# Kernel optimization log

Measured on AMD Instinct MI355X. Metric: run time of the kernel, lower is better.

The kernel has to match this reference:

```python
import jax, jax.numpy as jnp
import numpy as np

DIM = 1024
HEADS = 16
DIM_HEAD = 64
INNER = HEADS * DIM_HEAD  # 1024
SCALE = DIM_HEAD ** -0.5


def layernorm(x, gamma, beta, eps=1e-5):
    mu = jnp.mean(x, axis=-1, keepdims=True)
    var = jnp.var(x, axis=-1, keepdims=True)
    return (x - mu) * jax.lax.rsqrt(var + eps) * gamma + beta


def setup_inputs() -> dict:
    key = jax.random.key(0)
    ks = jax.random.split(key, 6)
    x = jax.random.normal(ks[0], (2, 2048, DIM), dtype=jnp.float32)
    # params (stored [in, out]; torch Linear does x @ W.T with W [out, in])
    w_q = jax.random.normal(ks[1], (DIM, INNER), dtype=jnp.float32) * (DIM ** -0.5)
    w_kv = jax.random.normal(ks[2], (DIM, 2 * INNER), dtype=jnp.float32) * (DIM ** -0.5)
    w_out = jax.random.normal(ks[3], (INNER, DIM), dtype=jnp.float32) * (INNER ** -0.5)
    b_out = jnp.zeros((DIM,), dtype=jnp.float32)
    gamma = jnp.ones((DIM,), dtype=jnp.float32)
    beta = jnp.zeros((DIM,), dtype=jnp.float32)
    return {"x": x, "w_q": w_q, "w_kv": w_kv, "w_out": w_out, "b_out": b_out,
            "gamma": gamma, "beta": beta}


def reference(x, w_q, w_kv, w_out, b_out, gamma, beta):
    b, n, _ = x.shape
    xn = layernorm(x, gamma, beta)
    q = xn @ w_q                           # [b, n, inner]
    kv = xn @ w_kv                         # [b, n, 2*inner]
    k, v = jnp.split(kv, 2, axis=-1)
    def split_heads(t):
        return t.reshape(b, n, HEADS, DIM_HEAD).transpose(0, 2, 1, 3)  # b h n d
    q, k, v = split_heads(q), split_heads(k), split_heads(v)
    dots = jnp.einsum('bhid,bhjd->bhij', q, k) * SCALE   # [b, h, n, n]
    attn = jax.nn.softmax(dots, axis=-1)
    out = jnp.einsum('bhij,bhjd->bhid', attn, v)          # [b, h, n, d]
    out = out.transpose(0, 2, 1, 3).reshape(b, n, INNER)  # b n (h d)
    return out @ w_out + b_out
```

## Files before the change

### kernel.cpp

```cpp
#include <hip/hip_runtime.h>

typedef unsigned short u16;
typedef u16   u16x8 __attribute__((ext_vector_type(8)));
typedef __bf16 bf16x8 __attribute__((ext_vector_type(8)));
typedef float f32x4 __attribute__((ext_vector_type(4)));
typedef float f32x2 __attribute__((ext_vector_type(2)));
typedef _Float16 f16x4 __attribute__((ext_vector_type(4)));
typedef _Float16 f16x8 __attribute__((ext_vector_type(8)));
typedef unsigned u32x2 __attribute__((ext_vector_type(2)));

__device__ __forceinline__ u16 f2b(float f){ __bf16 h=(__bf16)f; return __builtin_bit_cast(u16,h); }

__device__ __forceinline__ f32x4 mfma16(u16x8 a, u16x8 b, f32x4 c){
  return __builtin_amdgcn_mfma_f32_16x16x32_bf16(
      __builtin_bit_cast(bf16x8,a), __builtin_bit_cast(bf16x8,b), c, 0,0,0);
}

__device__ __forceinline__ void gl2lds16(const u16* g, u16* l){
  __builtin_amdgcn_global_load_lds((const __attribute__((address_space(1))) void*)g,
                                   (__attribute__((address_space(3))) void*)l, 16, 0, 0);
}

__global__ __launch_bounds__(256) void ln_kernel(const float* __restrict__ x,
                                                 const float* __restrict__ gamma,
                                                 const float* __restrict__ beta,
                                                 u16* __restrict__ xn){
  const int row = blockIdx.x, t = threadIdx.x;
  const float4 v = ((const float4*)(x + (size_t)row*1024))[t];
  float s  = v.x+v.y+v.z+v.w;
  float sq = v.x*v.x+v.y*v.y+v.z*v.z+v.w*v.w;
  for (int m=1;m<64;m<<=1){ s += __shfl_xor(s,m); sq += __shfl_xor(sq,m); }
  __shared__ float red[8];
  const int w=t>>6, l=t&63;
  if(l==0){ red[w]=s; red[4+w]=sq; }
  __syncthreads();
  const float S  = red[0]+red[1]+red[2]+red[3];
  const float SQ = red[4]+red[5]+red[6]+red[7];
  const float mu = S*(1.f/1024.f);
  const float var= SQ*(1.f/1024.f)-mu*mu;
  const float rs = rsqrtf(var+1e-5f);
  const float4 g4=((const float4*)gamma)[t], b4=((const float4*)beta)[t];
  u16 o0=f2b((v.x-mu)*rs*g4.x+b4.x);
  u16 o1=f2b((v.y-mu)*rs*g4.y+b4.y);
  u16 o2=f2b((v.z-mu)*rs*g4.z+b4.z);
  u16 o3=f2b((v.w-mu)*rs*g4.w+b4.w);
  uint2 p; p.x=(unsigned)o0|((unsigned)o1<<16); p.y=(unsigned)o2|((unsigned)o3<<16);
  ((uint2*)(xn + (size_t)row*1024))[t]=p;
}

__global__ __launch_bounds__(256) void wtrans_all_kernel(const float* __restrict__ wq,
    const float* __restrict__ wkv, const float* __restrict__ wout,
    u16* __restrict__ wqkvt, u16* __restrict__ woutt){
  __shared__ float tile[64][65];
  const int bx=blockIdx.x, t=threadIdx.x;
  const float* in; u16* out; int C, cxx;
  if(bx<16){ in=wq;  out=wqkvt;           C=1024; cxx=bx; }
  else if(bx<48){ in=wkv; out=wqkvt+1024*1024; C=2048; cxx=bx-16; }
  else { in=wout; out=woutt;             C=1024; cxx=bx-48; }
  const int R=1024;
  const int c0=cxx*64, r0=blockIdx.y*64;
  {
    const int r=t>>2, cc=t&3;
    const float* gp = in + (size_t)(r0+r)*C + c0 + cc*16;
    #pragma unroll
    for(int i=0;i<4;i++){
      float4 f=((const float4*)gp)[i];
      tile[r][cc*16+i*4+0]=f.x; tile[r][cc*16+i*4+1]=f.y;
      tile[r][cc*16+i*4+2]=f.z; tile[r][cc*16+i*4+3]=f.w;
    }
  }
  __syncthreads();
  const int c=t>>2, rc=t&3;
  u16x8 a,b;
  #pragma unroll
  for(int i=0;i<8;i++) a[i]=f2b(tile[rc*16+i][c]);
  #pragma unroll
  for(int i=0;i<8;i++) b[i]=f2b(tile[rc*16+8+i][c]);
  u16* op = out + (size_t)(c0+c)*R + r0 + rc*16;
  *(u16x8*)op=a; *(u16x8*)(op+8)=b;
}

__global__ __launch_bounds__(256) void vpack_kernel(const u16* __restrict__ kv,
                                                    u16* __restrict__ vp){
  __shared__ u16 tile[64][72];
  const int tok0=blockIdx.x*64, h=blockIdx.y, bb=blockIdx.z, t=threadIdx.x;
  {
    const int r=t>>2, cc=t&3;
    const u16* gp = kv + (size_t)(bb*2048 + tok0 + r)*2048 + 1024 + h*64 + cc*16;
    *(u16x8*)&tile[r][cc*16]   = *(const u16x8*)gp;
    *(u16x8*)&tile[r][cc*16+8] = *(const u16x8*)(gp+8);
  }
  __syncthreads();
  const int d=t&63, sl=t>>6;
  #pragma unroll
  for(int pass=0;pass<2;pass++){
    const int combo=pass*4+sl;
    const int j32l=combo>>2, qd=combo&3;
    u16 pk[8];
    #pragma unroll
    for(int tt=0;tt<2;tt++)
      #pragma unroll
      for(int rr=0;rr<4;rr++){
        const unsigned bits=((unsigned)tile[j32l*32+tt*16+qd*4+rr][d])<<16;
        const _Float16 hh=(_Float16)__builtin_bit_cast(float,bits);
        pk[tt*4+rr]=__builtin_bit_cast(u16,hh);
      }
    uint4 w4;
    w4.x=(unsigned)pk[0]|((unsigned)pk[1]<<16); w4.y=(unsigned)pk[2]|((unsigned)pk[3]<<16);
    w4.z=(unsigned)pk[4]|((unsigned)pk[5]<<16); w4.w=(unsigned)pk[6]|((unsigned)pk[7]<<16);
    *(uint4*)&vp[((((size_t)(bb*16+h))*64 + (tok0>>5) + j32l)*4 + qd)*512 + d*8]=w4;
  }
}

template<int MODE,int TM>
__global__ __launch_bounds__(256) void gemm_bt_kernel(const u16* __restrict__ A,
    const u16* __restrict__ Bt, u16* __restrict__ outQ, u16* __restrict__ outKV,
    float* __restrict__ outF, const float* __restrict__ bias, float scale,
    int M, int N, int K){
  constexpr int MT = TM/32;
  __shared__ u16 As[TM*64];
  __shared__ u16 Bs[128*64];
  const int t=threadIdx.x, w=t>>6, l=t&63, qd=l>>4, ln=l&15;
  const int m0=blockIdx.y*TM, n0=blockIdx.x*128;
  const int wm=(w>>1)*(TM/2), wn=(w&1)*64;
  f32x4 acc[MT][4] = {};
  const int nK = K>>6;
  for(int kt=0; kt<nK; kt++){
    const int k0=kt*64;
    #pragma unroll
    for(int p=0;p<MT;p++){
      const int cid=p*256+t, r=cid>>3, pc=cid&7, g=pc^(r&7);
      gl2lds16(A + (size_t)(m0+r)*K + k0 + g*8, &As[(p*256 + (t&192))*8]);
    }
    #pragma unroll
    for(int p=0;p<4;p++){
      const int cid=p*256+t, r=cid>>3, pc=cid&7, g=pc^(r&7);
      gl2lds16(Bt + (size_t)(n0+r)*K + k0 + g*8, &Bs[(p*256 + (t&192))*8]);
    }
    __syncthreads();
    #pragma unroll
    for(int ks=0;ks<2;ks++){
      u16x8 af[MT], bf[4];
      #pragma unroll
      for(int mt=0;mt<MT;mt++){
        const int m=wm+mt*16+ln, kc=ks*4+qd, pcc=kc^(m&7);
        af[mt]=*(const u16x8*)&As[m*64 + pcc*8];
      }
      #pragma unroll
      for(int nt=0;nt<4;nt++){
        const int n=wn+nt*16+ln, kc=ks*4+qd, pcc=kc^(n&7);
        bf[nt]=*(const u16x8*)&Bs[n*64 + pcc*8];
      }
      #pragma unroll
      for(int mt=0;mt<MT;mt++)
        #pragma unroll
        for(int nt=0;nt<4;nt++)
          acc[mt][nt]=mfma16(af[mt],bf[nt],acc[mt][nt]);
    }
    __syncthreads();
  }
  if(MODE==1){
    #pragma unroll
    for(int mt=0;mt<MT;mt++)
      #pragma unroll
      for(int rr=0;rr<4;rr++){
        const int row = m0+wm+mt*16+qd*4+rr;
        #pragma unroll
        for(int nt=0;nt<4;nt++){
          const int col = n0+wn+nt*16+ln;
          outF[(size_t)row*N+col]=acc[mt][nt][rr]+bias[col];
        }
      }
  } else {
    u16* outp; int ostr; float sc;
    if(n0<1024){ outp=outQ+n0; ostr=1024; sc=scale; }
    else       { outp=outKV+(n0-1024); ostr=2048; sc=1.f; }
    #pragma unroll
    for(int mt=0;mt<MT;mt++)
      #pragma unroll
      for(int rr=0;rr<4;rr++){
        const int row = m0+wm+mt*16+qd*4+rr;
        #pragma unroll
        for(int nt=0;nt<4;nt++)
          outp[(size_t)row*ostr + wn+nt*16+ln]=f2b(acc[mt][nt][rr]*sc);
      }
  }
}

__global__ __launch_bounds__(256,4) void attn_kernel(const u16* __restrict__ Q,
    const u16* __restrict__ Kb, const u16* __restrict__ Vp, u16* __restrict__ O){
  __shared__ u16 Ks[8192];
  __shared__ u16 Vs[8192];
  const int qt=blockIdx.x, h=blockIdx.y, bb=blockIdx.z;
  const int t=threadIdx.x, w=t>>6, l=t&63, qd=l>>4, ln=l&15;
  const int q0=qt*64;
  const size_t baseQ=(size_t)bb*2048*1024 + h*64;
  const size_t baseK=(size_t)bb*2048*2048 + h*64;
  const size_t baseV=(size_t)(bb*16+h)*131072;
  u16x8 qf[2];
  #pragma unroll
  for(int ks=0;ks<2;ks++)
    qf[ks] = *(const u16x8*)(Q + baseQ + (size_t)(q0+w*16+ln)*1024 + ks*32+qd*8);
  f32x2 l2={0.f,0.f};
  f32x4 o_acc[4]={};
  const f32x4 zf={0.f,0.f,0.f,0.f};

  for(int j0=0;j0<2048;j0+=128){
    __syncthreads();
    #pragma unroll
    for(int p=0;p<4;p++){
      const int r=(p*256+t)>>3, g=(t&7)^((t>>3)&7);
      gl2lds16(Kb + baseK + (size_t)(j0+r)*2048 + g*8, &Ks[(p*256+(t&192))*8]);
    }
    #pragma unroll
    for(int p=0;p<4;p++){
      gl2lds16(Vp + baseV + (size_t)(j0>>5)*2048 + (size_t)(p*256+t)*8,
               &Vs[(p*256+(t&192))*8]);
    }
    __syncthreads();

    #pragma unroll
    for(int jh=0;jh<2;jh++){
      f32x4 s[4];
      #pragma unroll
      for(int ks=0;ks<2;ks++){
        u16x8 kf[4];
        #pragma unroll
        for(int j4=0;j4<4;j4++){
          const int row=(jh*4+j4)*16+ln;
          kf[j4]=*(const u16x8*)&Ks[row*64 + (((ks*4+qd)^(ln&7))*8)];
        }
        #pragma unroll
        for(int j4=0;j4<4;j4++)
          s[j4] = ks? mfma16(kf[j4],qf[1],s[j4]) : mfma16(kf[j4],qf[0],zf);
      }
      #pragma unroll
      for(int al=0;al<2;al++){
        const int a=jh*2+al;
        f16x8 vf2[4];
        #pragma unroll
        for(int dt=0;dt<4;dt++)
          vf2[dt]=*(const f16x8*)&Vs[((a*4+qd)*64 + dt*16+ln)*8];
        #pragma unroll
        for(int tt=0;tt<2;tt++){
          const int j4l=al*2+tt;
          const float p0=exp2f(s[j4l][0]), p1=exp2f(s[j4l][1]);
          const float p2=exp2f(s[j4l][2]), p3=exp2f(s[j4l][3]);
          f32x2 pa; pa.x=p0; pa.y=p1;
          f32x2 pb; pb.x=p2; pb.y=p3;
          l2+=pa+pb;
          const auto lo=__builtin_amdgcn_cvt_pkrtz(p0,p1);
          const auto hi=__builtin_amdgcn_cvt_pkrtz(p2,p3);
          u32x2 pu; pu.x=__builtin_bit_cast(unsigned,lo); pu.y=__builtin_bit_cast(unsigned,hi);
          const f16x4 pf=__builtin_bit_cast(f16x4,pu);
          #pragma unroll
          for(int dt=0;dt<4;dt++){
            const f16x4 vf=tt? __builtin_shufflevector(vf2[dt],vf2[dt],4,5,6,7)
                             : __builtin_shufflevector(vf2[dt],vf2[dt],0,1,2,3);
            o_acc[dt]=__builtin_amdgcn_mfma_f32_16x16x16f16(pf,vf,o_acc[dt],0,0,0);
          }
        }
      }
    }
  }

  float li=l2.x+l2.y;
  li+=__shfl_xor(li,16);
  li+=__shfl_xor(li,32);
  const float linv=1.f/li;
  #pragma unroll
  for(int rr=0;rr<4;rr++){
    const float lr=__shfl(linv,qd*4+rr);
    const int row=q0+w*16+qd*4+rr;
    #pragma unroll
    for(int dt=0;dt<4;dt++)
      O[baseQ + (size_t)row*1024 + dt*16+ln]=f2b(o_acc[dt][rr]*lr);
  }
}

extern "C" void kernel_launch(void* const* d_in, const int* in_sizes, int n_in,
                              void* d_out, int out_size, void* d_ws, size_t ws_size,
                              hipStream_t stream) {
  const float* x     = (const float*)d_in[0];
  const float* w_q   = (const float*)d_in[1];
  const float* w_kv  = (const float*)d_in[2];
  const float* w_out = (const float*)d_in[3];
  const float* b_out = (const float*)d_in[4];
  const float* gamma = (const float*)d_in[5];
  const float* beta  = (const float*)d_in[6];
  float* out = (float*)d_out;

  char* ws=(char*)d_ws;
  size_t off=0;
  u16* xn    =(u16*)(ws+off); off += (size_t)4096*1024*2;
  u16* wqkvt =(u16*)(ws+off); off += (size_t)3072*1024*2;
  u16* woutt =(u16*)(ws+off); off += (size_t)1024*1024*2;
  u16* qb    =(u16*)(ws+off); off += (size_t)4096*1024*2;
  u16* kvb   =(u16*)(ws+off); off += (size_t)4096*2048*2;
  u16* vpb   =(u16*)(ws+off); off += (size_t)4096*1024*2;
  u16* ob    =(u16*)(ws+off); off += (size_t)4096*1024*2;

  ln_kernel<<<4096,256,0,stream>>>(x,gamma,beta,xn);
  wtrans_all_kernel<<<dim3(64,16),256,0,stream>>>(w_q,w_kv,w_out,wqkvt,woutt);

  const float SCALE_Q = 0.125f*1.4426950408889634f;
  gemm_bt_kernel<2,128><<<dim3(24,32),256,0,stream>>>(xn,wqkvt,qb,kvb,nullptr,nullptr,SCALE_Q,4096,3072,1024);
  vpack_kernel<<<dim3(32,16,2),256,0,stream>>>(kvb,vpb);
  attn_kernel<<<dim3(32,16,2),256,0,stream>>>(qb,kvb,vpb,ob);
  gemm_bt_kernel<1,64><<<dim3(8,64),256,0,stream>>>(ob,woutt,nullptr,nullptr,out,b_out,1.f,4096,1024,1024);
}
```

Baseline: 206.3 us.

## Fuse V packing into QKV GEMM epilogue and store K head-contiguous

```diff
diff --git a/kernel.cpp b/kernel.cpp
--- a/kernel.cpp
+++ b/kernel.cpp
@@ -80,43 +80,11 @@
   *(u16x8*)op=a; *(u16x8*)(op+8)=b;
 }
 
-__global__ __launch_bounds__(256) void vpack_kernel(const u16* __restrict__ kv,
-                                                    u16* __restrict__ vp){
-  __shared__ u16 tile[64][72];
-  const int tok0=blockIdx.x*64, h=blockIdx.y, bb=blockIdx.z, t=threadIdx.x;
-  {
-    const int r=t>>2, cc=t&3;
-    const u16* gp = kv + (size_t)(bb*2048 + tok0 + r)*2048 + 1024 + h*64 + cc*16;
-    *(u16x8*)&tile[r][cc*16]   = *(const u16x8*)gp;
-    *(u16x8*)&tile[r][cc*16+8] = *(const u16x8*)(gp+8);
-  }
-  __syncthreads();
-  const int d=t&63, sl=t>>6;
-  #pragma unroll
-  for(int pass=0;pass<2;pass++){
-    const int combo=pass*4+sl;
-    const int j32l=combo>>2, qd=combo&3;
-    u16 pk[8];
-    #pragma unroll
-    for(int tt=0;tt<2;tt++)
-      #pragma unroll
-      for(int rr=0;rr<4;rr++){
-        const unsigned bits=((unsigned)tile[j32l*32+tt*16+qd*4+rr][d])<<16;
-        const _Float16 hh=(_Float16)__builtin_bit_cast(float,bits);
-        pk[tt*4+rr]=__builtin_bit_cast(u16,hh);
-      }
-    uint4 w4;
-    w4.x=(unsigned)pk[0]|((unsigned)pk[1]<<16); w4.y=(unsigned)pk[2]|((unsigned)pk[3]<<16);
-    w4.z=(unsigned)pk[4]|((unsigned)pk[5]<<16); w4.w=(unsigned)pk[6]|((unsigned)pk[7]<<16);
-    *(uint4*)&vp[((((size_t)(bb*16+h))*64 + (tok0>>5) + j32l)*4 + qd)*512 + d*8]=w4;
-  }
-}
-
 template<int MODE,int TM>
 __global__ __launch_bounds__(256) void gemm_bt_kernel(const u16* __restrict__ A,
-    const u16* __restrict__ Bt, u16* __restrict__ outQ, u16* __restrict__ outKV,
-    float* __restrict__ outF, const float* __restrict__ bias, float scale,
-    int M, int N, int K){
+    const u16* __restrict__ Bt, u16* __restrict__ outQ, u16* __restrict__ outK,
+    u16* __restrict__ outV, float* __restrict__ outF, const float* __restrict__ bias,
+    float scale, int M, int N, int K){
   constexpr int MT = TM/32;
   __shared__ u16 As[TM*64];
   __shared__ u16 Bs[128*64];
@@ -171,10 +139,7 @@
           outF[(size_t)row*N+col]=acc[mt][nt][rr]+bias[col];
         }
       }
-  } else {
-    u16* outp; int ostr; float sc;
-    if(n0<1024){ outp=outQ+n0; ostr=1024; sc=scale; }
-    else       { outp=outKV+(n0-1024); ostr=2048; sc=1.f; }
+  } else if(n0<1024){
     #pragma unroll
     for(int mt=0;mt<MT;mt++)
       #pragma unroll
@@ -182,21 +147,47 @@
         const int row = m0+wm+mt*16+qd*4+rr;
         #pragma unroll
         for(int nt=0;nt<4;nt++)
-          outp[(size_t)row*ostr + wn+nt*16+ln]=f2b(acc[mt][nt][rr]*sc);
-      }
+          outQ[(size_t)row*1024 + n0+wn+nt*16+ln]=f2b(acc[mt][nt][rr]*scale);
+      }
+  } else if(n0<2048){
+    u16* kp = outK + (size_t)((m0>>11)*16 + ((n0-1024+wn)>>6))*131072;
+    const int jb = (m0&2047) + wm;
+    #pragma unroll
+    for(int mt=0;mt<MT;mt++)
+      #pragma unroll
+      for(int rr=0;rr<4;rr++){
+        const int j = jb + mt*16 + qd*4 + rr;
+        #pragma unroll
+        for(int nt=0;nt<4;nt++)
+          kp[(size_t)j*64 + nt*16+ln]=f2b(acc[mt][nt][rr]);
+      }
+  } else {
+    u16* vpp = outV + (size_t)((m0>>11)*16 + ((n0-2048+wn)>>6))*131072;
+    const int jb = (m0&2047) + wm;
+    #pragma unroll
+    for(int mt=0;mt<MT;mt++){
+      const int j = jb + mt*16 + qd*4;
+      const int vbase = ((j>>5)*4 + ((j>>2)&3))*512 + ((j>>4)&1)*4;
+      #pragma unroll
+      for(int nt=0;nt<4;nt++){
+        const auto lo=__builtin_amdgcn_cvt_pkrtz(acc[mt][nt][0],acc[mt][nt][1]);
+        const auto hi=__builtin_amdgcn_cvt_pkrtz(acc[mt][nt][2],acc[mt][nt][3]);
+        uint2 w2; w2.x=__builtin_bit_cast(unsigned,lo); w2.y=__builtin_bit_cast(unsigned,hi);
+        *(uint2*)&vpp[vbase + (nt*16+ln)*8] = w2;
+      }
+    }
   }
 }
 
 __global__ __launch_bounds__(256,4) void attn_kernel(const u16* __restrict__ Q,
-    const u16* __restrict__ Kb, const u16* __restrict__ Vp, u16* __restrict__ O){
+    const u16* __restrict__ Kp, const u16* __restrict__ Vp, u16* __restrict__ O){
   __shared__ u16 Ks[8192];
   __shared__ u16 Vs[8192];
   const int qt=blockIdx.x, h=blockIdx.y, bb=blockIdx.z;
   const int t=threadIdx.x, w=t>>6, l=t&63, qd=l>>4, ln=l&15;
   const int q0=qt*64;
   const size_t baseQ=(size_t)bb*2048*1024 + h*64;
-  const size_t baseK=(size_t)bb*2048*2048 + h*64;
-  const size_t baseV=(size_t)(bb*16+h)*131072;
+  const size_t baseKV=(size_t)(bb*16+h)*131072;
   u16x8 qf[2];
   #pragma unroll
   for(int ks=0;ks<2;ks++)
@@ -210,11 +201,11 @@
     #pragma unroll
     for(int p=0;p<4;p++){
       const int r=(p*256+t)>>3, g=(t&7)^((t>>3)&7);
-      gl2lds16(Kb + baseK + (size_t)(j0+r)*2048 + g*8, &Ks[(p*256+(t&192))*8]);
+      gl2lds16(Kp + baseKV + (size_t)(j0+r)*64 + g*8, &Ks[(p*256+(t&192))*8]);
     }
     #pragma unroll
     for(int p=0;p<4;p++){
-      gl2lds16(Vp + baseV + (size_t)(j0>>5)*2048 + (size_t)(p*256+t)*8,
+      gl2lds16(Vp + baseKV + (size_t)(j0>>5)*2048 + (size_t)(p*256+t)*8,
                &Vs[(p*256+(t&192))*8]);
     }
     __syncthreads();
@@ -296,7 +287,7 @@
   u16* wqkvt =(u16*)(ws+off); off += (size_t)3072*1024*2;
   u16* woutt =(u16*)(ws+off); off += (size_t)1024*1024*2;
   u16* qb    =(u16*)(ws+off); off += (size_t)4096*1024*2;
-  u16* kvb   =(u16*)(ws+off); off += (size_t)4096*2048*2;
+  u16* kpb   =(u16*)(ws+off); off += (size_t)4096*1024*2;
   u16* vpb   =(u16*)(ws+off); off += (size_t)4096*1024*2;
   u16* ob    =(u16*)(ws+off); off += (size_t)4096*1024*2;
 
@@ -304,8 +295,7 @@
   wtrans_all_kernel<<<dim3(64,16),256,0,stream>>>(w_q,w_kv,w_out,wqkvt,woutt);
 
   const float SCALE_Q = 0.125f*1.4426950408889634f;
-  gemm_bt_kernel<2,128><<<dim3(24,32),256,0,stream>>>(xn,wqkvt,qb,kvb,nullptr,nullptr,SCALE_Q,4096,3072,1024);
-  vpack_kernel<<<dim3(32,16,2),256,0,stream>>>(kvb,vpb);
-  attn_kernel<<<dim3(32,16,2),256,0,stream>>>(qb,kvb,vpb,ob);
-  gemm_bt_kernel<1,64><<<dim3(8,64),256,0,stream>>>(ob,woutt,nullptr,nullptr,out,b_out,1.f,4096,1024,1024);
-}
+  gemm_bt_kernel<2,128><<<dim3(24,32),256,0,stream>>>(xn,wqkvt,qb,kpb,vpb,nullptr,nullptr,SCALE_Q,4096,3072,1024);
+  attn_kernel<<<dim3(32,16,2),256,0,stream>>>(qb,kpb,vpb,ob);
+  gemm_bt_kernel<1,64><<<dim3(8,64),256,0,stream>>>(ob,woutt,nullptr,nullptr,nullptr,out,b_out,1.f,4096,1024,1024);
+}
```

Measured after the change: 197.3 us. 1.05x faster.
